# Optimization experiments

Measured on AMD Instinct MI355X. Metric: run time of the kernel, lower is better.

The kernel has to match this reference:

```python
import jax, jax.numpy as jnp
import numpy as np

N = 50000
E = 800000
HID = 128
EDGE_D = 1
NORM_FACTOR = 100.0


def setup_inputs() -> dict:
    key = jax.random.key(0)
    ks = jax.random.split(key, 12)
    in_dim = 2 * HID + EDGE_D  # 257
    # Xavier-uniform-ish init scales
    def xavier(k, shape, gain=1.0):
        fan_in, fan_out = shape[0], shape[1]
        a = gain * np.sqrt(6.0 / (fan_in + fan_out))
        return jax.random.uniform(k, shape, jnp.float32, -a, a)
    return {
        "h": jax.random.normal(ks[0], (N, HID), jnp.float32),
        "coord": jax.random.normal(ks[1], (N, 3), jnp.float32),
        "coord_diff": jax.random.normal(ks[2], (E, 3), jnp.float32),
        "coord_cross": jax.random.normal(ks[3], (E, 3), jnp.float32),
        "edge_attr": jax.random.normal(ks[4], (E, EDGE_D), jnp.float32),
        "edge_index": jax.random.randint(ks[5], (2, E), 0, N, jnp.int64),
        "W1": xavier(ks[6], (in_dim, HID)),
        "b1": jnp.zeros((HID,), jnp.float32),
        "W2": xavier(ks[7], (HID, HID)),
        "b2": jnp.zeros((HID,), jnp.float32),
        "W3": xavier(ks[8], (HID, 1), gain=0.001),
    }


def reference(h, coord, coord_diff, coord_cross, edge_attr, edge_index, W1, b1, W2, b2, W3):
    # reflection_equiv=True, tanh=False -> coord_cross unused, no tanh clamp
    row, col = edge_index[0], edge_index[1]
    # gather endpoint features and concat with edge attributes: [E, 2*HID+1]
    inp = jnp.concatenate([h[row], h[col], edge_attr], axis=1)
    x = jax.nn.silu(inp @ W1 + b1)
    x = jax.nn.silu(x @ W2 + b2)
    phi = x @ W3                      # [E, 1]
    trans = coord_diff * phi          # [E, 3]
    # unsorted_segment_sum over row with 'sum' aggregation (divide by norm factor)
    agg = jax.ops.segment_sum(trans, row, num_segments=coord.shape[0]) / NORM_FACTOR
    return coord + agg
```

## Files before the change

### kernel.cpp

```cpp
#include <hip/hip_runtime.h>
#include <stdint.h>

#define N_NODES 50000
#define E_EDGES 800000
#define HID 128
#define NGROUP 25000
#define BE 128
#define XS_STRIDE 264
#define YS_STRIDE 136
#define HS_STRIDE 132
#define CS_STRIDE 132

typedef unsigned short u16;
typedef unsigned char u8;
typedef __attribute__((ext_vector_type(8))) short svec8;
typedef __attribute__((ext_vector_type(16))) float fvec16;
typedef __attribute__((ext_vector_type(4))) unsigned uvec4;
typedef __attribute__((ext_vector_type(2))) unsigned uvec2;
typedef __attribute__((ext_vector_type(2))) float fvec2;

__device__ __forceinline__ float bf2f(u16 u) {
    union { unsigned int i; float f; } v; v.i = ((unsigned int)u) << 16; return v.f;
}
__device__ __forceinline__ u16 f2bf(float f) {
    union { float f; unsigned int i; } v; v.f = f;
    unsigned int u = v.i;
    return (u16)((u + 0x7fffu + ((u >> 16) & 1u)) >> 16);
}
__device__ __forceinline__ float lo16(unsigned u) {
    union { unsigned i; float f; } v; v.i = u << 16; return v.f;
}
__device__ __forceinline__ float hi16(unsigned u) {
    union { unsigned i; float f; } v; v.i = u & 0xFFFF0000u; return v.f;
}
__device__ __forceinline__ float silu_f(float x) {
    return x * __builtin_amdgcn_rcpf(1.0f + __expf(-x));
}
__device__ __forceinline__ float ldf(const void* p, size_t i, int is_bf) {
    return is_bf ? bf2f(((const u16*)p)[i]) : ((const float*)p)[i];
}
__device__ __forceinline__ int ldi(const void* p, size_t i, int is_i64) {
    return is_i64 ? ((const int*)p)[2 * i] : ((const int*)p)[i];
}

__device__ __forceinline__ void gld_lds16(const void* g, void* l) {
    __builtin_amdgcn_global_load_lds(
        (const __attribute__((address_space(1))) unsigned*)g,
        (__attribute__((address_space(3))) unsigned*)l, 16, 0, 0);
}

__device__ __forceinline__ int detect_bf_w(const void* p) {
    unsigned u = ((const u16*)p)[2 * (threadIdx.x & 63)];
    unsigned e = (u >> 7) & 0xFFu;
    unsigned long long m = __ballot(e >= 100u && e <= 140u);
    return __popcll(m) >= 48;
}
__device__ __forceinline__ int detect_i64_w(const void* eidx) {
    unsigned long long m = __ballot(((const int*)eidx)[2 * (threadIdx.x & 63) + 1] == 0);
    return __popcll(m) >= 48;
}

__global__ void transpose_w(const void* __restrict__ W1, const void* __restrict__ W2,
                            u16* __restrict__ W1t, u16* __restrict__ W2t,
                            u16* __restrict__ w1lb, float* __restrict__ agg) {
    const int is_bf = detect_bf_w(W1);
    int n = blockIdx.x;
    int k = threadIdx.x;
    W1t[n * 256 + k] = f2bf(ldf(W1, (size_t)k * 128 + n, is_bf));
    if (k < 128) W2t[n * 128 + k] = f2bf(ldf(W2, (size_t)k * 128 + n, is_bf));
    if (n == 0 && k < 128) w1lb[k] = f2bf(ldf(W1, (size_t)256 * 128 + k, is_bf));
    for (int i = blockIdx.x * 256 + k; i < N_NODES * 3; i += 128 * 256) agg[i] = 0.0f;
}

__global__ __launch_bounds__(256) void precompute_p(
    const void* __restrict__ h, const void* __restrict__ b1,
    const u16* __restrict__ W1t, u8* __restrict__ P)
{
    __shared__ __align__(16) union SMem {
        u16 Hs[64 * HS_STRIDE];
        float Cs[64 * CS_STRIDE];
    } sm;
    const int tid = threadIdx.x;
    const int is_bf = detect_bf_w(h);
    const int base = blockIdx.x * 64;
    {
        const int rr = tid >> 5, c = tid & 31;
        #pragma unroll
        for (int it = 0; it < 8; ++it) {
            int row = it * 8 + rr;
            int node = base + row; if (node > N_NODES - 1) node = N_NODES - 1;
            u16* dst = &sm.Hs[row * HS_STRIDE + c * 4];
            if (is_bf) {
                *(uint2*)dst = *(const uint2*)((const u16*)h + (size_t)node * HID + c * 4);
            } else {
                float4 v = *(const float4*)((const float*)h + (size_t)node * HID + c * 4);
                uint2 w;
                w.x = (unsigned)f2bf(v.x) | ((unsigned)f2bf(v.y) << 16);
                w.y = (unsigned)f2bf(v.z) | ((unsigned)f2bf(v.w) << 16);
                *(uint2*)dst = w;
            }
        }
    }
    __syncthreads();
    const int lane = tid & 63, wv = tid >> 6, l31 = lane & 31, hi = lane >> 5;
    const int mb = (wv & 1) * 32;
    const int tb = (wv >> 1) * 4;
    fvec16 acc[4] = {};
    for (int ks = 0; ks < 8; ++ks) {
        const int kk = ks * 16 + hi * 8;
        svec8 af = *(const svec8*)(&sm.Hs[(mb + l31) * HS_STRIDE + kk]);
        #pragma unroll
        for (int tt = 0; tt < 4; ++tt) {
            const int t = tb + tt;
            const int n = t * 32 + l31;
            const u16* bp = (t < 4) ? (W1t + n * 256 + kk)
                                    : (W1t + (n - 128) * 256 + 128 + kk);
            svec8 bf = *(const svec8*)bp;
            acc[tt] = __builtin_amdgcn_mfma_f32_32x32x16_bf16(af, bf, acc[tt], 0, 0, 0);
        }
    }
    __syncthreads();
    #pragma unroll
    for (int half = 0; half < 2; ++half) {
        if ((wv >> 1) == half) {
            #pragma unroll
            for (int tt = 0; tt < 4; ++tt) {
                const int colh = tt * 32 + l31;
                const float bias = (half == 0) ? ldf(b1, colh, is_bf) : 0.0f;
                #pragma unroll
                for (int r = 0; r < 16; ++r) {
                    int m = (r & 3) + 8 * (r >> 2) + 4 * hi;
                    sm.Cs[(mb + m) * CS_STRIDE + colh] = acc[tt][r] + bias;
                }
            }
        }
        __syncthreads();
        #pragma unroll
        for (int i = 0; i < 2; ++i) {
            int row = i * 32 + (tid >> 3);
            int node = base + row;
            if (node < N_NODES) {
                const float* src = &sm.Cs[row * CS_STRIDE + (tid & 7) * 16];
                uvec4 outv;
                #pragma unroll
                for (int d = 0; d < 4; ++d) {
                    int w = __builtin_amdgcn_cvt_pk_fp8_f32(src[d * 4 + 0], src[d * 4 + 1], 0, false);
                    w     = __builtin_amdgcn_cvt_pk_fp8_f32(src[d * 4 + 2], src[d * 4 + 3], w, true);
                    outv[d] = (unsigned)w;
                }
                *(uvec4*)(P + (size_t)node * 256 + half * 128 + (tid & 7) * 16) = outv;
            }
        }
        __syncthreads();
    }
}

__global__ __launch_bounds__(256, 2) void egnn_edge_p(
    const u8* __restrict__ P, const void* __restrict__ coord_diff,
    const void* __restrict__ edge_attr, const void* __restrict__ edge_index,
    const u16* __restrict__ w1lb, const void* __restrict__ b2,
    const void* __restrict__ W3, const u16* __restrict__ W2t,
    float* __restrict__ agg)
{
    __shared__ __align__(16) u8  W2f8[16384];
    __shared__ __align__(16) u8  PB[4][8192];
    __shared__ __align__(16) u16 w1ls[128];
    const int tid = threadIdx.x;
    #pragma unroll
    for (int i = 0; i < 8; ++i) {
        int f = i * 256 + tid;
        int t = f >> 9, ks = (f >> 6) & 7, fh = (f >> 5) & 1, fl = f & 31;
        svec8 v = *(const svec8*)(W2t + (t * 32 + fl) * 128 + fh * 64 + ks * 8);
        float x0 = bf2f((u16)v[0]), x1 = bf2f((u16)v[1]), x2 = bf2f((u16)v[2]), x3 = bf2f((u16)v[3]);
        float x4 = bf2f((u16)v[4]), x5 = bf2f((u16)v[5]), x6 = bf2f((u16)v[6]), x7 = bf2f((u16)v[7]);
        int w0 = __builtin_amdgcn_cvt_pk_fp8_f32(x0, x1, 0, false);
        w0     = __builtin_amdgcn_cvt_pk_fp8_f32(x2, x3, w0, true);
        int w1 = __builtin_amdgcn_cvt_pk_fp8_f32(x4, x5, 0, false);
        w1     = __builtin_amdgcn_cvt_pk_fp8_f32(x6, x7, w1, true);
        uvec2 wv2; wv2[0] = (unsigned)w0; wv2[1] = (unsigned)w1;
        *(uvec2*)(&W2f8[f * 8]) = wv2;
    }
    if (tid < 16) *(uvec4*)(&w1ls[tid * 8]) = *(const uvec4*)(w1lb + tid * 8);
    const int is_bf = detect_bf_w(edge_attr);
    const int is_i64 = detect_i64_w(edge_index);
    const int lane = tid & 63, wv = tid >> 6, l31 = lane & 31, hi = lane >> 5;

    float b2c[4], w3c[4];
    #pragma unroll
    for (int t = 0; t < 4; ++t) {
        int c = t * 32 + l31;
        b2c[t] = ldf(b2, c, is_bf);
        w3c[t] = ldf(W3, c, is_bf);
    }
    __syncthreads();

    u8* const pbw = &PB[wv][0];

    const int b0 = l31 & 1, bb1 = (l31 >> 1) & 1, bb2 = (l31 >> 2) & 1, bb3 = (l31 >> 3) & 1;
    const int rr = (b0 << 3) | (bb1 << 2) | (bb2 << 1) | bb3;
    const int em = (rr & 3) + 8 * (rr >> 2) + 4 * hi;

    const int wid = blockIdx.x * 4 + wv, nw = gridDim.x * 4;
    int g = wid;
    int rowN = 0, colN = 0; float eaN = 0.0f, ea_cur = 0.0f;
    {
        const int e = g * 32 + l31;
        const int row0 = ldi(edge_index, (size_t)e, is_i64);
        const int col0 = ldi(edge_index, (size_t)E_EDGES + e, is_i64);
        ea_cur = ldf(edge_attr, (size_t)e, is_bf);
        const u8* pr = P + (size_t)row0 * 256 + hi * 64;
        const u8* pc = P + (size_t)col0 * 256 + 128 + hi * 64;
        __builtin_amdgcn_sched_barrier(0);
        #pragma unroll
        for (int j = 0; j < 4; ++j) gld_lds16(pr + j * 16, pbw + j * 1024);
        #pragma unroll
        for (int j = 0; j < 4; ++j) gld_lds16(pc + j * 16, pbw + 4096 + j * 1024);
        __builtin_amdgcn_sched_barrier(0);
        const int gn = g + nw;
        const int en = gn * 32 + l31;
        rowN = ldi(edge_index, (size_t)en, is_i64);
        colN = ldi(edge_index, (size_t)E_EDGES + en, is_i64);
        eaN  = ldf(edge_attr, (size_t)en, is_bf);
    }
    while (g < NGROUP) {
        const int gn = g + nw;
        asm volatile("s_waitcnt vmcnt(3)" ::: "memory");
        uvec4 pv1[4], pv2[4];
        #pragma unroll
        for (int j = 0; j < 4; ++j) pv1[j] = *(const uvec4*)(pbw + j * 1024 + lane * 16);
        #pragma unroll
        for (int j = 0; j < 4; ++j) pv2[j] = *(const uvec4*)(pbw + 4096 + j * 1024 + lane * 16);
        long long af8[8];
        #pragma unroll
        for (int ks = 0; ks < 8; ++ks) {
            const unsigned a0 = pv1[ks >> 1][(ks & 1) * 2];
            const unsigned a1 = pv1[ks >> 1][(ks & 1) * 2 + 1];
            const unsigned c0 = pv2[ks >> 1][(ks & 1) * 2];
            const unsigned c1 = pv2[ks >> 1][(ks & 1) * 2 + 1];
            float q1[8], q2[8];
            {
                fvec2 t0 = __builtin_amdgcn_cvt_pk_f32_fp8((int)a0, false);
                fvec2 t1 = __builtin_amdgcn_cvt_pk_f32_fp8((int)a0, true);
                fvec2 t2 = __builtin_amdgcn_cvt_pk_f32_fp8((int)a1, false);
                fvec2 t3 = __builtin_amdgcn_cvt_pk_f32_fp8((int)a1, true);
                q1[0] = t0[0]; q1[1] = t0[1]; q1[2] = t1[0]; q1[3] = t1[1];
                q1[4] = t2[0]; q1[5] = t2[1]; q1[6] = t3[0]; q1[7] = t3[1];
                fvec2 s0 = __builtin_amdgcn_cvt_pk_f32_fp8((int)c0, false);
                fvec2 s1 = __builtin_amdgcn_cvt_pk_f32_fp8((int)c0, true);
                fvec2 s2 = __builtin_amdgcn_cvt_pk_f32_fp8((int)c1, false);
                fvec2 s3 = __builtin_amdgcn_cvt_pk_f32_fp8((int)c1, true);
                q2[0] = s0[0]; q2[1] = s0[1]; q2[2] = s1[0]; q2[3] = s1[1];
                q2[4] = s2[0]; q2[5] = s2[1]; q2[6] = s3[0]; q2[7] = s3[1];
            }
            const uvec4 wl = *(const uvec4*)(&w1ls[(hi * 8 + ks) * 8]);
            float y[8];
            #pragma unroll
            for (int p = 0; p < 4; ++p) {
                const unsigned uw = wl[p];
                float xl = q1[2 * p]     + q2[2 * p]     + ea_cur * lo16(uw);
                float xh = q1[2 * p + 1] + q2[2 * p + 1] + ea_cur * hi16(uw);
                y[2 * p] = silu_f(xl); y[2 * p + 1] = silu_f(xh);
            }
            int w0 = __builtin_amdgcn_cvt_pk_fp8_f32(y[0], y[1], 0, false);
            w0     = __builtin_amdgcn_cvt_pk_fp8_f32(y[2], y[3], w0, true);
            int w1 = __builtin_amdgcn_cvt_pk_fp8_f32(y[4], y[5], 0, false);
            w1     = __builtin_amdgcn_cvt_pk_fp8_f32(y[6], y[7], w1, true);
            af8[ks] = (long long)(((unsigned long long)(unsigned)w1 << 32) | (unsigned)w0);
        }
        int rowN2 = 0, colN2 = 0; float eaN2 = 0.0f;
        if (gn + nw < NGROUP) {
            const int en = (gn + nw) * 32 + l31;
            rowN2 = ldi(edge_index, (size_t)en, is_i64);
            colN2 = ldi(edge_index, (size_t)E_EDGES + en, is_i64);
            eaN2  = ldf(edge_attr, (size_t)en, is_bf);
        }
        const int eg = g * 32 + em;
        const int r2 = ldi(edge_index, (size_t)eg, is_i64);
        float cd0, cd1;
        if (l31 < 16) {
            cd0 = ldf(coord_diff, (size_t)eg * 3 + 0, is_bf);
            cd1 = ldf(coord_diff, (size_t)eg * 3 + 1, is_bf);
        } else {
            cd0 = ldf(coord_diff, (size_t)eg * 3 + 2, is_bf);
            cd1 = 0.0f;
        }
        __builtin_amdgcn_sched_barrier(0);
        if (gn < NGROUP) {
            const u8* pr = P + (size_t)rowN * 256 + hi * 64;
            const u8* pc = P + (size_t)colN * 256 + 128 + hi * 64;
            #pragma unroll
            for (int j = 0; j < 4; ++j) gld_lds16(pr + j * 16, pbw + j * 1024);
            #pragma unroll
            for (int j = 0; j < 4; ++j) gld_lds16(pc + j * 16, pbw + 4096 + j * 1024);
        }
        __builtin_amdgcn_sched_barrier(0);
        float s[16];
        #pragma unroll
        for (int r = 0; r < 16; ++r) s[r] = 0.0f;
        #pragma unroll
        for (int t = 0; t < 4; ++t) {
            fvec16 acc = {};
            #pragma unroll
            for (int ks = 0; ks < 8; ++ks) {
                union { uvec2 u; long long l; } bu;
                bu.u = *(const uvec2*)(&W2f8[((t * 8 + ks) * 2 + hi) * 256 + l31 * 8]);
                acc = __builtin_amdgcn_mfma_f32_32x32x16_fp8_fp8(af8[ks], bu.l, acc, 0, 0, 0);
            }
            #pragma unroll
            for (int r = 0; r < 16; ++r)
                s[r] += silu_f(acc[r] + b2c[t]) * w3c[t];
        }
        #pragma unroll
        for (int r = 0; r < 16; ++r) s[r] += __shfl_xor(s[r], 1);
        float w4[8];
        #pragma unroll
        for (int j = 0; j < 8; ++j) w4[j] = b0 ? s[j + 8] : s[j];
        #pragma unroll
        for (int j = 0; j < 8; ++j) w4[j] += __shfl_xor(w4[j], 2);
        float x4[4];
        #pragma unroll
        for (int j = 0; j < 4; ++j) x4[j] = bb1 ? w4[j + 4] : w4[j];
        #pragma unroll
        for (int j = 0; j < 4; ++j) x4[j] += __shfl_xor(x4[j], 4);
        float y2[2];
        y2[0] = bb2 ? x4[2] : x4[0];
        y2[1] = bb2 ? x4[3] : x4[1];
        y2[0] += __shfl_xor(y2[0], 8);
        y2[1] += __shfl_xor(y2[1], 8);
        float z = bb3 ? y2[1] : y2[0];
        z += __shfl_xor(z, 16);
        if (l31 < 16) {
            atomicAdd(&agg[r2 * 3 + 0], cd0 * z);
            atomicAdd(&agg[r2 * 3 + 1], cd1 * z);
        } else {
            atomicAdd(&agg[r2 * 3 + 2], cd0 * z);
        }
        g = gn; ea_cur = eaN;
        rowN = rowN2; colN = colN2; eaN = eaN2;
    }
}

__global__ __launch_bounds__(256, 2) void egnn_edge_kernel(
    const void* __restrict__ h, const void* __restrict__ coord_diff,
    const void* __restrict__ edge_attr, const void* __restrict__ edge_index,
    const void* __restrict__ W1, const void* __restrict__ b1,
    const void* __restrict__ b2, const void* __restrict__ W3,
    const u16* __restrict__ W1t, const u16* __restrict__ W2t,
    float* __restrict__ agg)
{
    __shared__ __align__(16) u16 Xs[BE * XS_STRIDE];
    __shared__ int   rows_s[BE];
    __shared__ int   cols_s[BE];
    __shared__ float ea_s[BE];
    __shared__ float b1_s[HID], b2_s[HID], w1l_s[HID], w3_s[HID];

    const int tid = threadIdx.x;
    const int e0  = blockIdx.x * BE;
    const int is_bf  = detect_bf_w(h);
    const int is_i64 = detect_i64_w(edge_index);

    if (tid < BE) {
        rows_s[tid] = ldi(edge_index, (size_t)(e0 + tid), is_i64);
        cols_s[tid] = ldi(edge_index, (size_t)(E_EDGES + e0 + tid), is_i64);
        ea_s[tid]   = ldf(edge_attr, (size_t)(e0 + tid), is_bf);
    }
    if (tid < HID) {
        b1_s[tid]  = ldf(b1, tid, is_bf);
        b2_s[tid]  = ldf(b2, tid, is_bf);
        w1l_s[tid] = ldf(W1, (size_t)256 * 128 + tid, is_bf);
        w3_s[tid]  = ldf(W3, tid, is_bf);
    }
    __syncthreads();
    {
        const int gg = tid >> 4, c = tid & 15;
        #pragma unroll
        for (int it = 0; it < 16; ++it) {
            int hr = it * 16 + gg;
            int e = hr >> 1, half = hr & 1;
            int src = half ? cols_s[e] : rows_s[e];
            svec8 v;
            if (is_bf) {
                v = *(const svec8*)((const u16*)h + (size_t)src * HID + c * 8);
            } else {
                const float* hf = (const float*)h + (size_t)src * HID + c * 8;
                float4 va = *(const float4*)hf;
                float4 vb = *(const float4*)(hf + 4);
                v[0] = (short)f2bf(va.x); v[1] = (short)f2bf(va.y);
                v[2] = (short)f2bf(va.z); v[3] = (short)f2bf(va.w);
                v[4] = (short)f2bf(vb.x); v[5] = (short)f2bf(vb.y);
                v[6] = (short)f2bf(vb.z); v[7] = (short)f2bf(vb.w);
            }
            *(svec8*)(&Xs[e * XS_STRIDE + half * 128 + c * 8]) = v;
        }
    }
    __syncthreads();
    const int lane = tid & 63;
    const int wv   = tid >> 6;
    const int l31  = lane & 31, hi = lane >> 5;
    const int col  = wv * 32 + l31;

    fvec16 acc[4] = {};
    for (int ks = 0; ks < 16; ++ks) {
        const int kk = ks * 16 + hi * 8;
        svec8 bfrag = *(const svec8*)(W1t + col * 256 + kk);
        #pragma unroll
        for (int mt = 0; mt < 4; ++mt) {
            svec8 afrag = *(const svec8*)(&Xs[(mt * 32 + l31) * XS_STRIDE + kk]);
            acc[mt] = __builtin_amdgcn_mfma_f32_32x32x16_bf16(afrag, bfrag, acc[mt], 0, 0, 0);
        }
    }
    __syncthreads();
    u16* Ys = Xs;
    #pragma unroll
    for (int mt = 0; mt < 4; ++mt)
        #pragma unroll
        for (int r = 0; r < 16; ++r) {
            int row = mt * 32 + (r & 3) + 8 * (r >> 2) + 4 * hi;
            float v = acc[mt][r] + ea_s[row] * w1l_s[col] + b1_s[col];
            Ys[row * YS_STRIDE + col] = f2bf(silu_f(v));
        }
    __syncthreads();
    fvec16 acc2[4] = {};
    for (int ks = 0; ks < 8; ++ks) {
        const int kk = ks * 16 + hi * 8;
        svec8 bfrag = *(const svec8*)(W2t + col * 128 + kk);
        #pragma unroll
        for (int mt = 0; mt < 4; ++mt) {
            svec8 afrag = *(const svec8*)(&Ys[(mt * 32 + l31) * YS_STRIDE + kk]);
            acc2[mt] = __builtin_amdgcn_mfma_f32_32x32x16_bf16(afrag, bfrag, acc2[mt], 0, 0, 0);
        }
    }
    __syncthreads();
    #pragma unroll
    for (int mt = 0; mt < 4; ++mt)
        #pragma unroll
        for (int r = 0; r < 16; ++r) {
            int row = mt * 32 + (r & 3) + 8 * (r >> 2) + 4 * hi;
            float v = acc2[mt][r] + b2_s[col];
            Ys[row * YS_STRIDE + col] = f2bf(silu_f(v));
        }
    __syncthreads();
    if (tid < BE) {
        const int e = tid;
        float phi = 0.0f;
        #pragma unroll
        for (int j = 0; j < 16; ++j) {
            svec8 x = *(const svec8*)(&Ys[e * YS_STRIDE + j * 8]);
            #pragma unroll
            for (int t = 0; t < 8; ++t)
                phi += bf2f((u16)x[t]) * w3_s[j * 8 + t];
        }
        const size_t ei = (size_t)(e0 + e);
        const int r = rows_s[e];
        atomicAdd(&agg[r * 3 + 0], ldf(coord_diff, ei * 3 + 0, is_bf) * phi);
        atomicAdd(&agg[r * 3 + 1], ldf(coord_diff, ei * 3 + 1, is_bf) * phi);
        atomicAdd(&agg[r * 3 + 2], ldf(coord_diff, ei * 3 + 2, is_bf) * phi);
    }
}

__global__ void finalize_kernel(const void* __restrict__ coord,
                                const float* __restrict__ agg,
                                void* __restrict__ out) {
    const int is_bf = detect_bf_w(coord);
    int i = blockIdx.x * blockDim.x + threadIdx.x;
    if (i < N_NODES * 3) {
        float v = ldf(coord, i, is_bf) + agg[i] * 0.01f;
        if (is_bf) ((u16*)out)[i] = f2bf(v);
        else       ((float*)out)[i] = v;
    }
}

extern "C" void kernel_launch(void* const* d_in, const int* in_sizes, int n_in,
                              void* d_out, int out_size, void* d_ws, size_t ws_size,
                              hipStream_t stream) {
    const void* h          = d_in[0];
    const void* coord      = d_in[1];
    const void* coord_diff = d_in[2];
    const void* edge_attr  = d_in[4];
    const void* edge_index = d_in[5];
    const void* W1 = d_in[6];
    const void* b1 = d_in[7];
    const void* W2 = d_in[8];
    const void* b2 = d_in[9];
    const void* W3 = d_in[10];

    char* ws    = (char*)d_ws;
    float* agg  = (float*)ws;
    u16* W1t    = (u16*)(ws + 600064);
    u16* W2t    = (u16*)(ws + 665600);
    u16* w1lb   = (u16*)(ws + 698432);
    u8* P       = (u8*)(ws + 698880);
    const size_t NEED = 698880 + (size_t)N_NODES * 256;

    transpose_w<<<dim3(128), dim3(256), 0, stream>>>(W1, W2, W1t, W2t, w1lb, agg);

    if (ws_size >= NEED) {
        precompute_p<<<dim3((N_NODES + 63) / 64), dim3(256), 0, stream>>>(
            h, b1, W1t, P);
        egnn_edge_p<<<dim3(768), dim3(256), 0, stream>>>(
            P, coord_diff, edge_attr, edge_index, w1lb, b2, W3, W2t, agg);
    } else {
        egnn_edge_kernel<<<dim3(E_EDGES / BE), dim3(256), 0, stream>>>(
            h, coord_diff, edge_attr, edge_index, W1, b1, b2, W3, W1t, W2t, agg);
    }
    finalize_kernel<<<dim3((N_NODES * 3 + 255) / 256), dim3(256), 0, stream>>>(coord, agg, d_out);
}
```

Before: 239.0 us.

## Replicate aggregation buffer per block group and hoist LDS tile reads earlier

Each block now atomically accumulates into one of eight replicated agg buffers chosen by block index, and finalize sums the replicas. The goal is to reduce atomic contention on shared node addresses. The per-wave LDS reads of the next edge group's P rows move from the loop top to before the reduction/atomic phase, using a full vmcnt wait, so LDS latency overlaps the shuffle reductions. The cost is extra zeroing and read traffic for the replicas and a stricter wait on outstanding loads.

```diff
diff --git a/kernel.cpp b/kernel.cpp
--- a/kernel.cpp
+++ b/kernel.cpp
@@ -10,6 +10,7 @@
 #define YS_STRIDE 136
 #define HS_STRIDE 132
 #define CS_STRIDE 132
+#define AGG_STRIDE_F 150016
 
 typedef unsigned short u16;
 typedef unsigned char u8;
@@ -62,14 +63,14 @@
 
 __global__ void transpose_w(const void* __restrict__ W1, const void* __restrict__ W2,
                             u16* __restrict__ W1t, u16* __restrict__ W2t,
-                            u16* __restrict__ w1lb, float* __restrict__ agg) {
+                            u16* __restrict__ w1lb, float* __restrict__ agg, int nzero) {
     const int is_bf = detect_bf_w(W1);
     int n = blockIdx.x;
     int k = threadIdx.x;
     W1t[n * 256 + k] = f2bf(ldf(W1, (size_t)k * 128 + n, is_bf));
     if (k < 128) W2t[n * 128 + k] = f2bf(ldf(W2, (size_t)k * 128 + n, is_bf));
     if (n == 0 && k < 128) w1lb[k] = f2bf(ldf(W1, (size_t)256 * 128 + k, is_bf));
-    for (int i = blockIdx.x * 256 + k; i < N_NODES * 3; i += 128 * 256) agg[i] = 0.0f;
+    for (int i = blockIdx.x * 256 + k; i < nzero; i += 128 * 256) agg[i] = 0.0f;
 }
 
 __global__ __launch_bounds__(256) void precompute_p(
@@ -160,7 +161,7 @@
     const void* __restrict__ edge_attr, const void* __restrict__ edge_index,
     const u16* __restrict__ w1lb, const void* __restrict__ b2,
     const void* __restrict__ W3, const u16* __restrict__ W2t,
-    float* __restrict__ agg)
+    float* __restrict__ agg, int rep_mask)
 {
     __shared__ __align__(16) u8  W2f8[16384];
     __shared__ __align__(16) u8  PB[4][8192];
@@ -195,6 +196,7 @@
     __syncthreads();
 
     u8* const pbw = &PB[wv][0];
+    float* const aggw = agg + (size_t)(blockIdx.x & rep_mask) * AGG_STRIDE_F;
 
     const int b0 = l31 & 1, bb1 = (l31 >> 1) & 1, bb2 = (l31 >> 2) & 1, bb3 = (l31 >> 3) & 1;
     const int rr = (b0 << 3) | (bb1 << 2) | (bb2 << 1) | bb3;
@@ -203,6 +205,7 @@
     const int wid = blockIdx.x * 4 + wv, nw = gridDim.x * 4;
     int g = wid;
     int rowN = 0, colN = 0; float eaN = 0.0f, ea_cur = 0.0f;
+    uvec4 pv1[4], pv2[4];
     {
         const int e = g * 32 + l31;
         const int row0 = ldi(edge_index, (size_t)e, is_i64);
@@ -221,15 +224,14 @@
         rowN = ldi(edge_index, (size_t)en, is_i64);
         colN = ldi(edge_index, (size_t)E_EDGES + en, is_i64);
         eaN  = ldf(edge_attr, (size_t)en, is_bf);
+        asm volatile("s_waitcnt vmcnt(0)" ::: "memory");
+        #pragma unroll
+        for (int j = 0; j < 4; ++j) pv1[j] = *(const uvec4*)(pbw + j * 1024 + lane * 16);
+        #pragma unroll
+        for (int j = 0; j < 4; ++j) pv2[j] = *(const uvec4*)(pbw + 4096 + j * 1024 + lane * 16);
     }
     while (g < NGROUP) {
         const int gn = g + nw;
-        asm volatile("s_waitcnt vmcnt(3)" ::: "memory");
-        uvec4 pv1[4], pv2[4];
-        #pragma unroll
-        for (int j = 0; j < 4; ++j) pv1[j] = *(const uvec4*)(pbw + j * 1024 + lane * 16);
-        #pragma unroll
-        for (int j = 0; j < 4; ++j) pv2[j] = *(const uvec4*)(pbw + 4096 + j * 1024 + lane * 16);
         long long af8[8];
         #pragma unroll
         for (int ks = 0; ks < 8; ++ks) {
@@ -310,6 +312,13 @@
             for (int r = 0; r < 16; ++r)
                 s[r] += silu_f(acc[r] + b2c[t]) * w3c[t];
         }
+        if (gn < NGROUP) {
+            asm volatile("s_waitcnt vmcnt(0)" ::: "memory");
+            #pragma unroll
+            for (int j = 0; j < 4; ++j) pv1[j] = *(const uvec4*)(pbw + j * 1024 + lane * 16);
+            #pragma unroll
+            for (int j = 0; j < 4; ++j) pv2[j] = *(const uvec4*)(pbw + 4096 + j * 1024 + lane * 16);
+        }
         #pragma unroll
         for (int r = 0; r < 16; ++r) s[r] += __shfl_xor(s[r], 1);
         float w4[8];
@@ -330,10 +339,10 @@
         float z = bb3 ? y2[1] : y2[0];
         z += __shfl_xor(z, 16);
         if (l31 < 16) {
-            atomicAdd(&agg[r2 * 3 + 0], cd0 * z);
-            atomicAdd(&agg[r2 * 3 + 1], cd1 * z);
+            atomicAdd(&aggw[r2 * 3 + 0], cd0 * z);
+            atomicAdd(&aggw[r2 * 3 + 1], cd1 * z);
         } else {
-            atomicAdd(&agg[r2 * 3 + 2], cd0 * z);
+            atomicAdd(&aggw[r2 * 3 + 2], cd0 * z);
         }
         g = gn; ea_cur = eaN;
         rowN = rowN2; colN = colN2; eaN = eaN2;
@@ -460,11 +469,13 @@
 
 __global__ void finalize_kernel(const void* __restrict__ coord,
                                 const float* __restrict__ agg,
-                                void* __restrict__ out) {
+                                void* __restrict__ out, int rep) {
     const int is_bf = detect_bf_w(coord);
     int i = blockIdx.x * blockDim.x + threadIdx.x;
     if (i < N_NODES * 3) {
-        float v = ldf(coord, i, is_bf) + agg[i] * 0.01f;
+        float a = 0.0f;
+        for (int k = 0; k < rep; ++k) a += agg[(size_t)k * AGG_STRIDE_F + i];
+        float v = ldf(coord, i, is_bf) + a * 0.01f;
         if (is_bf) ((u16*)out)[i] = f2bf(v);
         else       ((float*)out)[i] = v;
     }
@@ -484,24 +495,31 @@
     const void* b2 = d_in[9];
     const void* W3 = d_in[10];
 
+    const size_t P_BYTES = (size_t)N_NODES * 256;
+    const size_t NEED8 = 8ull * 600064 + 98560 + P_BYTES;
+    const size_t NEED1 = 1ull * 600064 + 98560 + P_BYTES;
+
+    const int rep = (ws_size >= NEED8) ? 8 : 1;
     char* ws    = (char*)d_ws;
     float* agg  = (float*)ws;
-    u16* W1t    = (u16*)(ws + 600064);
-    u16* W2t    = (u16*)(ws + 665600);
-    u16* w1lb   = (u16*)(ws + 698432);
-    u8* P       = (u8*)(ws + 698880);
-    const size_t NEED = 698880 + (size_t)N_NODES * 256;
-
-    transpose_w<<<dim3(128), dim3(256), 0, stream>>>(W1, W2, W1t, W2t, w1lb, agg);
-
-    if (ws_size >= NEED) {
+    size_t a0   = (size_t)rep * 600064;
+    u16* W1t    = (u16*)(ws + a0);
+    u16* W2t    = (u16*)(ws + a0 + 65536);
+    u16* w1lb   = (u16*)(ws + a0 + 98304);
+    u8* P       = (u8*)(ws + a0 + 98560);
+
+    transpose_w<<<dim3(128), dim3(256), 0, stream>>>(W1, W2, W1t, W2t, w1lb, agg,
+                                                     rep * AGG_STRIDE_F);
+
+    if (ws_size >= (rep == 8 ? NEED8 : NEED1)) {
         precompute_p<<<dim3((N_NODES + 63) / 64), dim3(256), 0, stream>>>(
             h, b1, W1t, P);
         egnn_edge_p<<<dim3(768), dim3(256), 0, stream>>>(
-            P, coord_diff, edge_attr, edge_index, w1lb, b2, W3, W2t, agg);
+            P, coord_diff, edge_attr, edge_index, w1lb, b2, W3, W2t, agg, rep - 1);
     } else {
         egnn_edge_kernel<<<dim3(E_EDGES / BE), dim3(256), 0, stream>>>(
             h, coord_diff, edge_attr, edge_index, W1, b1, b2, W3, W1t, W2t, agg);
     }
-    finalize_kernel<<<dim3((N_NODES * 3 + 255) / 256), dim3(256), 0, stream>>>(coord, agg, d_out);
-}
+    finalize_kernel<<<dim3((N_NODES * 3 + 255) / 256), dim3(256), 0, stream>>>(
+        coord, agg, d_out, rep);
+}
```

After: 244.4 us. 2.3% more time.
